# Kernel optimization log

Measured on AMD Instinct MI355X. Metric: run time of the kernel, lower is better.

## Reference

```python
import jax, jax.numpy as jnp
import numpy as np

# Dimensions: N batch, Cin/Cout channels, T frames, V=25 joints, S=3 adjacency subsets
N, CIN, COUT, T, V, S = 128, 64, 64, 256, 25, 3
RED = COUT // 16            # SCE reduction channels
KER = V                     # V=25 is odd -> ker_jpt = 25, pad = 12
PAD = (KER - 1) // 2
BN_EPS = 1e-5


def setup_inputs() -> dict:
    key = jax.random.key(0)
    ks = jax.random.split(key, 12)
    x = jax.random.normal(ks[0], (N, CIN, T, V), dtype=jnp.float32)
    # fixed graph adjacency (3 subsets) and learnable PA (init: stacked identity)
    A = jax.random.uniform(ks[1], (S, V, V), dtype=jnp.float32) * (1.0 / V)
    PA = jnp.tile(jnp.eye(V, dtype=jnp.float32)[None], (S, 1, 1))
    # per-subset 1x1 conv weights [S, Cout, Cin] and biases
    wd = jax.random.normal(ks[2], (S, COUT, CIN), dtype=jnp.float32) * np.sqrt(2.0 / (COUT * S))
    bd = jnp.zeros((S, COUT), dtype=jnp.float32)
    # BatchNorm2d (inference: running stats)
    bn_gamma = jax.random.uniform(ks[3], (COUT,), dtype=jnp.float32) + 0.5
    bn_beta = jax.random.normal(ks[4], (COUT,), dtype=jnp.float32) * 0.1
    bn_mean = jax.random.normal(ks[5], (COUT,), dtype=jnp.float32) * 0.1
    bn_var = jax.random.uniform(ks[6], (COUT,), dtype=jnp.float32) + 0.5
    # SCE: conv_spatial (Conv1d Cout->RED, kernel 25, pad 12), conv_expand (1x1 RED->Cout)
    sce_ws = jax.random.normal(ks[7], (RED, COUT, KER), dtype=jnp.float32) * np.sqrt(2.0 / (COUT * KER))
    sce_bs = jnp.zeros((RED,), dtype=jnp.float32)
    sce_we = jax.random.normal(ks[8], (COUT, RED), dtype=jnp.float32) * np.sqrt(2.0 / RED)
    sce_be = jnp.zeros((COUT,), dtype=jnp.float32)
    return {"x": x, "A": A, "PA": PA, "wd": wd, "bd": bd,
            "bn_gamma": bn_gamma, "bn_beta": bn_beta, "bn_mean": bn_mean, "bn_var": bn_var,
            "sce_ws": sce_ws, "sce_bs": sce_bs, "sce_we": sce_we, "sce_be": sce_be}


def reference(x, A, PA, wd, bd, bn_gamma, bn_beta, bn_mean, bn_var,
              sce_ws, sce_bs, sce_we, sce_be):
    # L2_norm over dim=1 of PA (per subset, per column), then A = A + PA_norm
    pa_norm = jnp.sqrt(jnp.sum(PA * PA, axis=1, keepdims=True)) + 1e-4
    Af = A + PA / pa_norm                                   # [S, V, V]
    # sum_i conv1x1_i( x.view(N,CT,V) @ A[i] ): single fused contraction
    y = jnp.einsum('nctv,svw,soc->notw', x, Af, wd)
    y = y + jnp.sum(bd, axis=0)[None, :, None, None]        # [N, Cout, T, V]
    # BatchNorm2d (inference)
    scale = bn_gamma / jnp.sqrt(bn_var + BN_EPS)
    y = y * scale[None, :, None, None] + (bn_beta - bn_mean * scale)[None, :, None, None]
    # residual (in_channels == out_channels -> identity down) + ReLU
    y = jax.nn.relu(y + x)
    # SCE: temporal avg-pool -> conv1d over joints -> relu -> 1x1 expand -> sigmoid gate
    p = jnp.mean(y, axis=2)                                 # [N, Cout, V]
    s = jax.lax.conv_general_dilated(
        p, sce_ws, window_strides=(1,), padding=[(PAD, PAD)],
        dimension_numbers=('NCH', 'OIH', 'NCH')) + sce_bs[None, :, None]
    s = jax.nn.relu(s)                                      # [N, RED, V]
    g = jax.nn.sigmoid(jnp.einsum('nrv,or->nov', s, sce_we) + sce_be[None, :, None])
    # x * sigmoid(g) + x
    return y * (g[:, :, None, :] + 1.0)
```

## Files before the change

kernel.cpp:

```cpp
#include <hip/hip_runtime.h>
#include <hip/hip_bf16.h>

typedef __attribute__((ext_vector_type(8))) short short8;
typedef __attribute__((ext_vector_type(4))) short shortx4;
typedef __attribute__((ext_vector_type(4))) float floatx4;

#define NB   128
#define TT   256
#define TW   4
#define X_N  409600
#define X_C  6400

#define WS_P     0
#define WS_GATE  204800
#define WS_B2    409600
#define WS_AFB   409664
#define WS_W2B   410944

static __device__ __forceinline__ ushort f2b(float f) {
    union { __hip_bfloat16 h; ushort u; } c;
    c.h = __float2bfloat16(f);
    return c.u;
}
static __device__ __forceinline__ float b2f(ushort u) {
    union { ushort u; __hip_bfloat16 h; } c;
    c.u = u;
    return __bfloat162float(c.h);
}

__global__ __launch_bounds__(256) void prep_kernel(
    const float* __restrict__ A, const float* __restrict__ PA,
    const float* __restrict__ wd, const float* __restrict__ bd,
    const float* __restrict__ gamma, const float* __restrict__ beta,
    const float* __restrict__ mean, const float* __restrict__ var,
    float* __restrict__ bias2, ushort* __restrict__ Afb, ushort* __restrict__ W2b)
{
    __shared__ float norms[75];
    __shared__ float scs[64];
    int tid = threadIdx.x;
    if (tid < 75) {
        int s = tid / 25, w = tid - s * 25;
        float acc = 0.f;
        for (int i = 0; i < 25; ++i) {
            float v = PA[s * 625 + i * 25 + w];
            acc += v * v;
        }
        norms[tid] = sqrtf(acc) + 1e-4f;
    }
    if (tid < 64) {
        float sc = gamma[tid] * rsqrtf(var[tid] + 1e-5f);
        scs[tid] = sc;
        float bsum = bd[tid] + bd[64 + tid] + bd[128 + tid];
        bias2[tid] = bsum * sc + beta[tid] - mean[tid] * sc;
    }
    __syncthreads();
    for (int i = tid; i < 2560; i += 256) {
        int j = i & 7; int lane = (i >> 3) & 63; int nt = i >> 9;
        int scol = nt * 16 + (lane & 15);
        int v = ((lane >> 4) & 3) * 8 + j;
        float val = 0.f;
        if (scol < 75 && v < 25) {
            int s = scol / 25, w = scol - s * 25;
            int idx = s * 625 + v * 25 + w;
            val = A[idx] + PA[idx] / norms[s * 25 + w];
        }
        Afb[i] = f2b(val);
    }
    for (int i = tid; i < 12288; i += 256) {
        int j = i & 7; int lane = (i >> 3) & 63; int kq = i >> 9;
        int k = kq % 6; int ot = kq / 6;
        int o = ot * 16 + (lane & 15);
        int kk = k * 32 + ((lane >> 4) & 3) * 8 + j;
        int s = kk >> 6, c = kk & 63;
        W2b[i] = f2b(wd[s * 4096 + o * 64 + c] * scs[o]);
    }
}

__global__ __launch_bounds__(256, 2) void main_kernel(
    const float* __restrict__ x, const ushort* __restrict__ Afb,
    const ushort* __restrict__ W2b, const float* __restrict__ bias2,
    float* __restrict__ yout, float* __restrict__ p)
{
    __shared__ ushort xs[4 * 64 * 36];
    __shared__ ushort zb[112 * 200];

    int blk = blockIdx.x;
    int n = blk >> 6, tb = blk & 63, t0 = tb * TW;
    int tid = threadIdx.x;
    int q = tid >> 6, lane = tid & 63, lm = lane & 15, quad = lane >> 4;

    short8 bfr[5];
    #pragma unroll
    for (int nt = 0; nt < 5; ++nt)
        bfr[nt] = *(const short8*)(Afb + (nt * 64 + lane) * 8);
    short8 wf[6];
    #pragma unroll
    for (int k = 0; k < 6; ++k)
        wf[k] = *(const short8*)(W2b + ((q * 6 + k) * 64 + lane) * 8);
    floatx4 bias = *(const floatx4*)(bias2 + q * 16 + quad * 4);

    const float* xn = x + (size_t)n * X_N + t0 * 25;
    for (int i = tid; i < 6400; i += 256) {
        int c = i / 100, r = i - c * 100;
        int t = r / 25, v = r - t * 25;
        xs[(t * 64 + c) * 36 + v] = f2b(xn[c * X_C + r]);
    }
    for (int i = tid; i < 1792; i += 256) {
        int c = i / 28, rr = i - c * 28;
        int t = rr / 7, v = 25 + (rr - t * 7);
        xs[(t * 64 + c) * 36 + v] = 0;
    }
    __syncthreads();

    {
        const int t = q;
        #pragma unroll
        for (int cm = 0; cm < 4; ++cm) {
            const ushort* ap = &xs[(t * 64 + cm * 16 + lm) * 36 + quad * 8];
            shortx4 a0 = *(const shortx4*)ap;
            shortx4 a1 = *(const shortx4*)(ap + 4);
            short8 av = __builtin_shufflevector(a0, a1, 0, 1, 2, 3, 4, 5, 6, 7);
            #pragma unroll
            for (int nt = 0; nt < 5; ++nt) {
                floatx4 d = __builtin_amdgcn_mfma_f32_16x16x32_bf16(
                    av, bfr[nt], (floatx4)(0.f), 0, 0, 0);
                int scol = nt * 16 + lm;
                if (scol < 75) {
                    int s = scol / 25, w = scol - s * 25;
                    int zcol = t * 25 + w;
                    int krow = s * 64 + cm * 16 + quad * 4;
                    shortx4 sv;
                    sv.x = (short)f2b(d.x); sv.y = (short)f2b(d.y);
                    sv.z = (short)f2b(d.z); sv.w = (short)f2b(d.w);
                    *(shortx4*)(&zb[zcol * 200 + krow]) = sv;
                }
            }
        }
    }
    __syncthreads();

    floatx4 acc[7];
    #pragma unroll
    for (int nt = 0; nt < 7; ++nt) acc[nt] = (floatx4)(0.f);
    #pragma unroll
    for (int k = 0; k < 6; ++k) {
        #pragma unroll
        for (int nt = 0; nt < 7; ++nt) {
            int col = nt * 16 + lm;
            short8 b = *(const short8*)(&zb[col * 200 + k * 32 + quad * 8]);
            acc[nt] = __builtin_amdgcn_mfma_f32_16x16x32_bf16(wf[k], b, acc[nt], 0, 0, 0);
        }
    }
    __syncthreads();

    float* ypool = (float*)zb;
    for (int i = tid; i < 1600; i += 256) ypool[i] = 0.f;
    __syncthreads();

    int o0 = q * 16 + quad * 4;
    #pragma unroll
    for (int nt = 0; nt < 7; ++nt) {
        int col = nt * 16 + lm;
        if (col < 100) {
            int t = col / 25, w = col - t * 25;
            size_t base = (size_t)n * X_N + (size_t)o0 * X_C + (size_t)(t0 + t) * 25 + w;
            #pragma unroll
            for (int r = 0; r < 4; ++r) {
                float res = b2f(xs[(t * 64 + o0 + r) * 36 + w]);
                float vv = acc[nt][r] + bias[r] + res;
                vv = fmaxf(vv, 0.f);
                yout[base + (size_t)r * X_C] = vv;
                atomicAdd(&ypool[(o0 + r) * 25 + w], vv);
            }
        }
    }
    __syncthreads();
    for (int i = tid; i < 1600; i += 256)
        atomicAdd(&p[(size_t)n * 1600 + i], ypool[i]);
}

__global__ __launch_bounds__(256) void sce_kernel(
    const float* __restrict__ p, const float* __restrict__ sws,
    const float* __restrict__ sbs, const float* __restrict__ swe,
    const float* __restrict__ sbe, float* __restrict__ gate)
{
    __shared__ float pm[1600];
    __shared__ float wss[6400];
    __shared__ float sq[100];
    int n = blockIdx.x, tid = threadIdx.x;
    for (int i = tid; i < 1600; i += 256) pm[i] = p[n * 1600 + i] * (1.f / 256.f);
    for (int i = tid; i < 6400; i += 256) wss[i] = sws[i];
    __syncthreads();
    if (tid < 100) {
        int r = tid / 25, w = tid - (tid / 25) * 25;
        float acc = sbs[r];
        for (int o = 0; o < 64; ++o) {
            const float* wr = &wss[(r * 64 + o) * 25];
            const float* pr = &pm[o * 25];
            int k0 = (w < 12) ? 12 - w : 0;
            int k1 = (w > 12) ? 37 - w : 25;
            for (int k = k0; k < k1; ++k) acc += pr[w + k - 12] * wr[k];
        }
        sq[tid] = fmaxf(acc, 0.f);
    }
    __syncthreads();
    for (int i = tid; i < 1600; i += 256) {
        int o = i / 25, w = i - (i / 25) * 25;
        float acc = sbe[o];
        #pragma unroll
        for (int r = 0; r < 4; ++r) acc += sq[r * 25 + w] * swe[o * 4 + r];
        gate[n * 1600 + i] = 1.f + 1.f / (1.f + __expf(-acc));
    }
}

__global__ __launch_bounds__(256) void gate_mul_kernel(
    float* __restrict__ y, const float* __restrict__ gate)
{
    unsigned int i = (blockIdx.x * 256u + threadIdx.x) * 4u;
    float4 v = *(float4*)(y + i);
    unsigned int i1 = i + 1, i2 = i + 2, i3 = i + 3;
    float g0 = gate[(i  / 6400u) * 25u + (i  % 25u)];
    float g1 = gate[(i1 / 6400u) * 25u + (i1 % 25u)];
    float g2 = gate[(i2 / 6400u) * 25u + (i2 % 25u)];
    float g3 = gate[(i3 / 6400u) * 25u + (i3 % 25u)];
    v.x *= g0; v.y *= g1; v.z *= g2; v.w *= g3;
    *(float4*)(y + i) = v;
}

extern "C" void kernel_launch(void* const* d_in, const int* in_sizes, int n_in,
                              void* d_out, int out_size, void* d_ws, size_t ws_size,
                              hipStream_t stream) {
    const float* x     = (const float*)d_in[0];
    const float* A     = (const float*)d_in[1];
    const float* PA    = (const float*)d_in[2];
    const float* wd    = (const float*)d_in[3];
    const float* bd    = (const float*)d_in[4];
    const float* gamma = (const float*)d_in[5];
    const float* beta  = (const float*)d_in[6];
    const float* mean  = (const float*)d_in[7];
    const float* var   = (const float*)d_in[8];
    const float* sws   = (const float*)d_in[9];
    const float* sbs   = (const float*)d_in[10];
    const float* swe   = (const float*)d_in[11];
    const float* sbe   = (const float*)d_in[12];

    float* out   = (float*)d_out;
    float* ws    = (float*)d_ws;
    float* p     = ws + WS_P;
    float* gate  = ws + WS_GATE;
    float* bias2 = ws + WS_B2;
    ushort* Afb  = (ushort*)(ws + WS_AFB);
    ushort* W2b  = (ushort*)(ws + WS_W2B);

    hipMemsetAsync(p, 0, 204800 * sizeof(float), stream);

    prep_kernel<<<1, 256, 0, stream>>>(A, PA, wd, bd, gamma, beta, mean, var,
                                       bias2, Afb, W2b);
    main_kernel<<<NB * (TT / TW), 256, 0, stream>>>(x, Afb, W2b, bias2, out, p);
    sce_kernel<<<NB, 256, 0, stream>>>(p, sws, sbs, swe, sbe, gate);
    gate_mul_kernel<<<out_size / (256 * 4), 256, 0, stream>>>(out, gate);
}
```

Measured before the change: 786.4 us.

## Split main kernel across 8 waves, stage output in LDS, replace atomic pooling with partials

```diff
diff --git a/kernel.cpp b/kernel.cpp
--- a/kernel.cpp
+++ b/kernel.cpp
@@ -11,11 +11,11 @@
 #define X_N  409600
 #define X_C  6400
 
-#define WS_P     0
-#define WS_GATE  204800
-#define WS_B2    409600
-#define WS_AFB   409664
-#define WS_W2B   410944
+#define WS_GATE  0
+#define WS_B2    204800
+#define WS_AFB   204864
+#define WS_W2B   206144
+#define WS_PART  212288
 
 static __device__ __forceinline__ ushort f2b(float f) {
     union { __hip_bfloat16 h; ushort u; } c;
@@ -38,6 +38,7 @@
     __shared__ float norms[75];
     __shared__ float scs[64];
     int tid = threadIdx.x;
+    int gid = blockIdx.x * 256 + tid;
     if (tid < 75) {
         int s = tid / 25, w = tid - s * 25;
         float acc = 0.f;
@@ -50,11 +51,13 @@
     if (tid < 64) {
         float sc = gamma[tid] * rsqrtf(var[tid] + 1e-5f);
         scs[tid] = sc;
-        float bsum = bd[tid] + bd[64 + tid] + bd[128 + tid];
-        bias2[tid] = bsum * sc + beta[tid] - mean[tid] * sc;
-    }
-    __syncthreads();
-    for (int i = tid; i < 2560; i += 256) {
+        if (blockIdx.x == 0) {
+            float bsum = bd[tid] + bd[64 + tid] + bd[128 + tid];
+            bias2[tid] = bsum * sc + beta[tid] - mean[tid] * sc;
+        }
+    }
+    __syncthreads();
+    for (int i = gid; i < 2560; i += 4096) {
         int j = i & 7; int lane = (i >> 3) & 63; int nt = i >> 9;
         int scol = nt * 16 + (lane & 15);
         int v = ((lane >> 4) & 3) * 8 + j;
@@ -66,7 +69,7 @@
         }
         Afb[i] = f2b(val);
     }
-    for (int i = tid; i < 12288; i += 256) {
+    for (int i = gid; i < 12288; i += 4096) {
         int j = i & 7; int lane = (i >> 3) & 63; int kq = i >> 9;
         int k = kq % 6; int ot = kq / 6;
         int o = ot * 16 + (lane & 15);
@@ -76,18 +79,21 @@
     }
 }
 
-__global__ __launch_bounds__(256, 2) void main_kernel(
+template<bool PART>
+__global__ __launch_bounds__(512, 4) void main_kernel(
     const float* __restrict__ x, const ushort* __restrict__ Afb,
     const ushort* __restrict__ W2b, const float* __restrict__ bias2,
-    float* __restrict__ yout, float* __restrict__ p)
+    float* __restrict__ yout, float* __restrict__ part)
 {
     __shared__ ushort xs[4 * 64 * 36];
     __shared__ ushort zb[112 * 200];
+    float* ypf = (float*)zb;
 
     int blk = blockIdx.x;
     int n = blk >> 6, tb = blk & 63, t0 = tb * TW;
     int tid = threadIdx.x;
-    int q = tid >> 6, lane = tid & 63, lm = lane & 15, quad = lane >> 4;
+    int w8 = tid >> 6, lane = tid & 63, lm = lane & 15, quad = lane >> 4;
+    int ot = w8 & 3, h = w8 >> 2;
 
     short8 bfr[5];
     #pragma unroll
@@ -96,16 +102,16 @@
     short8 wf[6];
     #pragma unroll
     for (int k = 0; k < 6; ++k)
-        wf[k] = *(const short8*)(W2b + ((q * 6 + k) * 64 + lane) * 8);
-    floatx4 bias = *(const floatx4*)(bias2 + q * 16 + quad * 4);
+        wf[k] = *(const short8*)(W2b + ((ot * 6 + k) * 64 + lane) * 8);
+    floatx4 bias = *(const floatx4*)(bias2 + ot * 16 + quad * 4);
 
     const float* xn = x + (size_t)n * X_N + t0 * 25;
-    for (int i = tid; i < 6400; i += 256) {
+    for (int i = tid; i < 6400; i += 512) {
         int c = i / 100, r = i - c * 100;
         int t = r / 25, v = r - t * 25;
         xs[(t * 64 + c) * 36 + v] = f2b(xn[c * X_C + r]);
     }
-    for (int i = tid; i < 1792; i += 256) {
+    for (int i = tid; i < 1792; i += 512) {
         int c = i / 28, rr = i - c * 28;
         int t = rr / 7, v = 25 + (rr - t * 7);
         xs[(t * 64 + c) * 36 + v] = 0;
@@ -113,9 +119,10 @@
     __syncthreads();
 
     {
-        const int t = q;
+        const int t = w8 & 3;
         #pragma unroll
-        for (int cm = 0; cm < 4; ++cm) {
+        for (int cj = 0; cj < 2; ++cj) {
+            int cm = h * 2 + cj;
             const ushort* ap = &xs[(t * 64 + cm * 16 + lm) * 36 + quad * 8];
             shortx4 a0 = *(const shortx4*)ap;
             shortx4 a1 = *(const shortx4*)(ap + 4);
@@ -139,48 +146,83 @@
     }
     __syncthreads();
 
-    floatx4 acc[7];
-    #pragma unroll
-    for (int nt = 0; nt < 7; ++nt) acc[nt] = (floatx4)(0.f);
+    floatx4 acc[4];
+    int nt0 = h * 4;
+    #pragma unroll
+    for (int j = 0; j < 4; ++j) acc[j] = bias;
     #pragma unroll
     for (int k = 0; k < 6; ++k) {
         #pragma unroll
-        for (int nt = 0; nt < 7; ++nt) {
+        for (int j = 0; j < 4; ++j) {
+            int nt = nt0 + j;
+            if (nt < 7) {
+                int col = nt * 16 + lm;
+                short8 b = *(const short8*)(&zb[col * 200 + k * 32 + quad * 8]);
+                acc[j] = __builtin_amdgcn_mfma_f32_16x16x32_bf16(wf[k], b, acc[j], 0, 0, 0);
+            }
+        }
+    }
+    __syncthreads();
+
+    int o0 = ot * 16 + quad * 4;
+    #pragma unroll
+    for (int j = 0; j < 4; ++j) {
+        int nt = nt0 + j;
+        if (nt < 7) {
             int col = nt * 16 + lm;
-            short8 b = *(const short8*)(&zb[col * 200 + k * 32 + quad * 8]);
-            acc[nt] = __builtin_amdgcn_mfma_f32_16x16x32_bf16(wf[k], b, acc[nt], 0, 0, 0);
-        }
-    }
-    __syncthreads();
-
-    float* ypool = (float*)zb;
-    for (int i = tid; i < 1600; i += 256) ypool[i] = 0.f;
-    __syncthreads();
-
-    int o0 = q * 16 + quad * 4;
-    #pragma unroll
-    for (int nt = 0; nt < 7; ++nt) {
-        int col = nt * 16 + lm;
-        if (col < 100) {
-            int t = col / 25, w = col - t * 25;
-            size_t base = (size_t)n * X_N + (size_t)o0 * X_C + (size_t)(t0 + t) * 25 + w;
-            #pragma unroll
-            for (int r = 0; r < 4; ++r) {
-                float res = b2f(xs[(t * 64 + o0 + r) * 36 + w]);
-                float vv = acc[nt][r] + bias[r] + res;
-                vv = fmaxf(vv, 0.f);
-                yout[base + (size_t)r * X_C] = vv;
-                atomicAdd(&ypool[(o0 + r) * 25 + w], vv);
+            if (col < 100) {
+                #pragma unroll
+                for (int r = 0; r < 4; ++r)
+                    ypf[(o0 + r) * 100 + col] = acc[j][r];
             }
         }
     }
     __syncthreads();
-    for (int i = tid; i < 1600; i += 256)
-        atomicAdd(&p[(size_t)n * 1600 + i], ypool[i]);
-}
-
+
+    size_t ybase = (size_t)n * X_N + (size_t)tb * 100;
+    for (int j = tid; j < 6400; j += 512) {
+        int o = j / 100, rr = j - o * 100;
+        int t = rr / 25, w = rr - t * 25;
+        float v = ypf[j] + b2f(xs[(t * 64 + o) * 36 + w]);
+        v = fmaxf(v, 0.f);
+        yout[ybase + (size_t)o * X_C + rr] = v;
+        if (PART) ypf[j] = v;
+    }
+    if (PART) {
+        __syncthreads();
+        for (int i = tid; i < 1600; i += 512) {
+            int o = i / 25, w = i - o * 25;
+            const float* yp = &ypf[o * 100 + w];
+            part[(size_t)blk * 1600 + i] = yp[0] + yp[25] + yp[50] + yp[75];
+        }
+    }
+}
+
+__global__ __launch_bounds__(256) void pool_kernel(
+    const float* __restrict__ y, float* __restrict__ p)
+{
+    __shared__ float red[8][25];
+    int no = blockIdx.x;
+    int tid = threadIdx.x;
+    if (tid < 200) {
+        int tg = tid / 25, w = tid - tg * 25;
+        const float* yp = y + (size_t)no * 6400 + w;
+        float s = 0.f;
+        for (int t = tg * 32; t < tg * 32 + 32; ++t) s += yp[t * 25];
+        red[tg][w] = s;
+    }
+    __syncthreads();
+    if (tid < 25) {
+        float s = 0.f;
+        #pragma unroll
+        for (int g = 0; g < 8; ++g) s += red[g][tid];
+        p[(size_t)no * 25 + tid] = s;
+    }
+}
+
+template<bool PART>
 __global__ __launch_bounds__(256) void sce_kernel(
-    const float* __restrict__ p, const float* __restrict__ sws,
+    const float* __restrict__ pp, const float* __restrict__ sws,
     const float* __restrict__ sbs, const float* __restrict__ swe,
     const float* __restrict__ sbe, float* __restrict__ gate)
 {
@@ -188,7 +230,17 @@
     __shared__ float wss[6400];
     __shared__ float sq[100];
     int n = blockIdx.x, tid = threadIdx.x;
-    for (int i = tid; i < 1600; i += 256) pm[i] = p[n * 1600 + i] * (1.f / 256.f);
+    if (PART) {
+        for (int i = tid; i < 1600; i += 256) {
+            const float* q = pp + (size_t)n * 64 * 1600 + i;
+            float s = 0.f;
+            for (int tb = 0; tb < 64; ++tb) s += q[(size_t)tb * 1600];
+            pm[i] = s * (1.f / 256.f);
+        }
+    } else {
+        for (int i = tid; i < 1600; i += 256)
+            pm[i] = pp[(size_t)n * 1600 + i] * (1.f / 256.f);
+    }
     for (int i = tid; i < 6400; i += 256) wss[i] = sws[i];
     __syncthreads();
     if (tid < 100) {
@@ -209,7 +261,7 @@
         float acc = sbe[o];
         #pragma unroll
         for (int r = 0; r < 4; ++r) acc += sq[r * 25 + w] * swe[o * 4 + r];
-        gate[n * 1600 + i] = 1.f + 1.f / (1.f + __expf(-acc));
+        gate[(size_t)n * 1600 + i] = 1.f + 1.f / (1.f + __expf(-acc));
     }
 }
 
@@ -246,17 +298,23 @@
 
     float* out   = (float*)d_out;
     float* ws    = (float*)d_ws;
-    float* p     = ws + WS_P;
     float* gate  = ws + WS_GATE;
     float* bias2 = ws + WS_B2;
     ushort* Afb  = (ushort*)(ws + WS_AFB);
     ushort* W2b  = (ushort*)(ws + WS_W2B);
-
-    hipMemsetAsync(p, 0, 204800 * sizeof(float), stream);
-
-    prep_kernel<<<1, 256, 0, stream>>>(A, PA, wd, bd, gamma, beta, mean, var,
-                                       bias2, Afb, W2b);
-    main_kernel<<<NB * (TT / TW), 256, 0, stream>>>(x, Afb, W2b, bias2, out, p);
-    sce_kernel<<<NB, 256, 0, stream>>>(p, sws, sbs, swe, sbe, gate);
+    float* part  = ws + WS_PART;
+
+    bool useA = ws_size >= ((size_t)WS_PART + (size_t)8192 * 1600) * 4;
+
+    prep_kernel<<<16, 256, 0, stream>>>(A, PA, wd, bd, gamma, beta, mean, var,
+                                        bias2, Afb, W2b);
+    if (useA) {
+        main_kernel<true><<<NB * (TT / TW), 512, 0, stream>>>(x, Afb, W2b, bias2, out, part);
+        sce_kernel<true><<<NB, 256, 0, stream>>>(part, sws, sbs, swe, sbe, gate);
+    } else {
+        main_kernel<false><<<NB * (TT / TW), 512, 0, stream>>>(x, Afb, W2b, bias2, out, part);
+        pool_kernel<<<NB * 64, 256, 0, stream>>>(out, part);
+        sce_kernel<false><<<NB, 256, 0, stream>>>(part, sws, sbs, swe, sbe, gate);
+    }
     gate_mul_kernel<<<out_size / (256 * 4), 256, 0, stream>>>(out, gate);
 }
```

After: 740.5 us. -5.8%, faster.
